# Kernel tuning notes

Hardware: AMD Instinct MI355X
Metric: run time of the kernel (lower is better)

## Reference

```python
import jax, jax.numpy as jnp
import numpy as np
from math import sqrt

N = 50000
E = 800000
D_EMB = 512
DK = 64
DV = 64
HEADS = 8


def setup_inputs() -> dict:
    key = jax.random.key(0)
    k1, k2, k3, k4 = jax.random.split(key, 4)
    x = jax.random.normal(k1, (N, D_EMB), dtype=jnp.float32)
    edge_index = jax.random.randint(k2, (2, E), 0, N, dtype=jnp.int64)
    out_qkv = (2 * DK + DV) * HEADS  # 1536
    W_qkv = jax.random.normal(k3, (out_qkv, D_EMB), dtype=jnp.float32) / sqrt(D_EMB)
    b_qkv = jnp.zeros((out_qkv,), dtype=jnp.float32)
    W_ff = jax.random.normal(k4, (D_EMB, DV * HEADS), dtype=jnp.float32) / sqrt(DV * HEADS)
    b_ff = jnp.zeros((D_EMB,), dtype=jnp.float32)
    return {"x": x, "edge_index": edge_index, "W_qkv": W_qkv, "b_qkv": b_qkv,
            "W_ff": W_ff, "b_ff": b_ff}


def _attention_message(Q, K, V, senders, receivers, n_nodes):
    # Q,K: [N, H, dK], V: [N, H, dV]; edge lists: [E]
    scale = 1.0 / sqrt(Q.shape[-1])
    # per-edge scores: [E, H]
    scores = jnp.einsum('ehd,ehd->eh', Q[receivers], K[senders]) * scale
    # segment softmax over incoming edges of each receiver
    smax = jax.ops.segment_max(scores, receivers, num_segments=n_nodes)  # [N, H]
    ex = jnp.exp(scores - smax[receivers])                               # [E, H]
    denom = jax.ops.segment_sum(ex, receivers, num_segments=n_nodes)    # [N, H]
    att = ex / denom[receivers]                                         # [E, H]
    # weighted scatter of V from senders to receivers: [N, H, dV]
    out = jax.ops.segment_sum(att[:, :, None] * V[senders], receivers,
                              num_segments=n_nodes)
    return out, att


def reference(x, edge_index, W_qkv, b_qkv, W_ff, b_ff):
    n_nodes = x.shape[0]
    qkv = x @ W_qkv.T + b_qkv  # [N, (2*dK+dV)*H]
    Q, K, V = jnp.split(qkv, [DK * HEADS, 2 * DK * HEADS], axis=-1)
    Q = Q.reshape(n_nodes, HEADS, DK)
    K = K.reshape(n_nodes, HEADS, DK)
    V = V.reshape(n_nodes, HEADS, DV)
    senders, receivers = edge_index[0], edge_index[1]
    msg, _ = _attention_message(Q, K, V, senders, receivers, n_nodes)
    # aggregate_heads: flatten heads and project to d_Embedding
    out = msg.reshape(n_nodes, HEADS * DV) @ W_ff.T + b_ff
    return out
```

## Files before the change

kernel.cpp:

```cpp
#include <hip/hip_runtime.h>

static constexpr int NN = 50000;
static constexpr int NE = 800000;
static constexpr int DEMB = 512;
static constexpr int QKV_OUT = 1536;

typedef _Float16 half8 __attribute__((ext_vector_type(8)));
typedef float floatx4 __attribute__((ext_vector_type(4)));

#define KQ_SCALE (127.0f / 5.5f)
#define KQ_DEQ   (5.5f / 127.0f)

static constexpr size_t OFF_QH   = 0;
static constexpr size_t OFF_VH   = 51200000;
static constexpr size_t OFF_K8   = 102400000;
static constexpr size_t OFF_MSG  = 153600000;
static constexpr size_t OFF_SRT  = 204800000;
static constexpr size_t OFF_DEG  = 208000000;
static constexpr size_t OFF_OFFA = 208200000;
static constexpr size_t OFF_CUR  = 208400064;
static constexpr size_t OFF_FLAG = 208600064;
static constexpr size_t OFF_WQH  = 208600128;
static constexpr size_t OFF_WFH  = 210172992;

typedef __attribute__((address_space(1))) const void* gas_ptr;
typedef __attribute__((address_space(3))) void* lds_ptr_t;

__device__ __forceinline__ void load_lds16(const void* g, void* l) {
  __builtin_amdgcn_global_load_lds((gas_ptr)g, (lds_ptr_t)l, 16, 0, 0);
}

__global__ __launch_bounds__(256)
void k_cvt(const float* __restrict__ in, _Float16* __restrict__ out, int n8) {
  int i = blockIdx.x * 256 + threadIdx.x;
  if (i < n8) {
    floatx4 a = *(const floatx4*)(in + (size_t)i * 8);
    floatx4 b = *(const floatx4*)(in + (size_t)i * 8 + 4);
    half8 h;
    #pragma unroll
    for (int q = 0; q < 4; ++q) { h[q] = (_Float16)a[q]; h[q + 4] = (_Float16)b[q]; }
    *(half8*)(out + (size_t)i * 8) = h;
  }
}

__global__ __launch_bounds__(64)
void k_detect64(const void* __restrict__ edge, int* __restrict__ flag) {
  if (threadIdx.x == 0) {
    const int* p = (const int*)edge;
    int is64 = 1;
    for (int i = 0; i < 16; ++i) if (p[2 * i + 1] != 0) is64 = 0;
    *flag = is64;
  }
}

__device__ __forceinline__ int edge_at(const void* edge, int row, int e, int is64) {
  if (is64) return (int)((const long long*)edge)[(size_t)row * NE + e];
  return ((const int*)edge)[(size_t)row * NE + e];
}

__global__ __launch_bounds__(256)
void k_histo(const void* __restrict__ edge, const int* __restrict__ flag,
             int* __restrict__ deg) {
  int e = blockIdx.x * 256 + threadIdx.x;
  if (e < NE) {
    int r = edge_at(edge, 1, e, *flag);
    atomicAdd(&deg[r], 1);
  }
}

__global__ __launch_bounds__(1024)
void k_scan(const int* __restrict__ deg, int* __restrict__ off,
            int* __restrict__ cur, int n) {
  __shared__ int sums[1024];
  int tid = threadIdx.x;
  int per = (n + 1023) >> 10;
  int start = tid * per;
  int end = start + per; if (end > n) end = n;
  int s = 0;
  for (int i = start; i < end; ++i) s += deg[i];
  sums[tid] = s;
  __syncthreads();
  for (int d = 1; d < 1024; d <<= 1) {
    int v = (tid >= d) ? sums[tid - d] : 0;
    __syncthreads();
    sums[tid] += v;
    __syncthreads();
  }
  int run = (tid == 0) ? 0 : sums[tid - 1];
  for (int i = start; i < end; ++i) {
    off[i] = run; cur[i] = run; run += deg[i];
  }
  if (tid == 0) off[n] = sums[1023];
}

__global__ __launch_bounds__(256)
void k_scatter(const void* __restrict__ edge, const int* __restrict__ flag,
               int* __restrict__ cur, int* __restrict__ srt) {
  int e = blockIdx.x * 256 + threadIdx.x;
  if (e < NE) {
    int is64 = *flag;
    int r = edge_at(edge, 1, e, is64);
    int s = edge_at(edge, 0, e, is64);
    int pos = atomicAdd(&cur[r], 1);
    srt[pos] = s;
  }
}

template<int MODE>
__global__ __launch_bounds__(256)
void k_gemm_nt(const _Float16* __restrict__ Ah, const _Float16* __restrict__ Bh,
               const float* __restrict__ bias,
               void* __restrict__ out0, void* __restrict__ out1, void* __restrict__ out2,
               int M, int N, int K) {
  __shared__ _Float16 As[128 * 32];
  __shared__ _Float16 Bs[128 * 32];
  const int tid = threadIdx.x;
  const int m0 = blockIdx.x * 128;
  const int n0 = blockIdx.y * 128;
  const int wid = tid >> 6, lane = tid & 63;
  const int wr = wid >> 1, wc = wid & 1;

  floatx4 acc[4][4];
  #pragma unroll
  for (int i = 0; i < 4; ++i)
    #pragma unroll
    for (int j = 0; j < 4; ++j)
      #pragma unroll
      for (int q = 0; q < 4; ++q) acc[i][j][q] = 0.f;

  const int srow = tid >> 2;
  const int sslot = tid & 3;
  const int fr = lane & 15;
  const int fslot = lane >> 4;

  int garow0 = m0 + srow;       if (garow0 >= M) garow0 = M - 1;
  int garow1 = m0 + srow + 64;  if (garow1 >= M) garow1 = M - 1;
  const int aslot0 = sslot ^ (srow & 3);
  const int gbrow0 = n0 + srow, gbrow1 = n0 + srow + 64;

  for (int k0 = 0; k0 < K; k0 += 32) {
    load_lds16(Ah + (size_t)garow0 * K + k0 + aslot0 * 8, (char*)As + wid * 1024);
    load_lds16(Ah + (size_t)garow1 * K + k0 + aslot0 * 8, (char*)As + 4096 + wid * 1024);
    load_lds16(Bh + (size_t)gbrow0 * K + k0 + aslot0 * 8, (char*)Bs + wid * 1024);
    load_lds16(Bh + (size_t)gbrow1 * K + k0 + aslot0 * 8, (char*)Bs + 4096 + wid * 1024);
    __syncthreads();

    half8 a[4], b[4];
    #pragma unroll
    for (int m = 0; m < 4; ++m) {
      int R = wr * 64 + m * 16 + fr;
      a[m] = *(const half8*)(As + R * 32 + ((fslot ^ (R & 3)) << 3));
    }
    #pragma unroll
    for (int n = 0; n < 4; ++n) {
      int R = wc * 64 + n * 16 + fr;
      b[n] = *(const half8*)(Bs + R * 32 + ((fslot ^ (R & 3)) << 3));
    }
    #pragma unroll
    for (int m = 0; m < 4; ++m)
      #pragma unroll
      for (int n = 0; n < 4; ++n)
        acc[m][n] = __builtin_amdgcn_mfma_f32_16x16x32_f16(a[m], b[n], acc[m][n], 0, 0, 0);
    __syncthreads();
  }

  const int fq = (lane >> 4) << 2;
  #pragma unroll
  for (int m = 0; m < 4; ++m) {
    #pragma unroll
    for (int n = 0; n < 4; ++n) {
      int gn = n0 + wc * 64 + n * 16 + fr;
      float bv = bias[gn];
      #pragma unroll
      for (int q = 0; q < 4; ++q) {
        int gm = m0 + wr * 64 + m * 16 + fq + q;
        if (gm < M) {
          float val = acc[m][n][q] + bv;
          if (MODE == 0) {
            int region = gn >> 9;
            int col = gn & 511;
            size_t idx = (size_t)gm * 512 + col;
            if (region == 0)      ((_Float16*)out0)[idx] = (_Float16)val;
            else if (region == 1) {
              float s = fminf(fmaxf(val * KQ_SCALE, -127.f), 127.f);
              ((signed char*)out1)[idx] = (signed char)__float2int_rn(s);
            }
            else                  ((_Float16*)out2)[idx] = (_Float16)val;
          } else {
            ((float*)out0)[(size_t)gm * N + gn] = val;
          }
        }
      }
    }
  }
}

__global__ __launch_bounds__(256)
void k_attn(const _Float16* __restrict__ Qh, const signed char* __restrict__ K8,
            const _Float16* __restrict__ Vh, const int* __restrict__ off,
            const int* __restrict__ srt, _Float16* __restrict__ msg) {
  int r = blockIdx.x * 4 + (threadIdx.x >> 6);
  if (r >= NN) return;
  int lane = threadIdx.x & 63;
  int h = lane >> 3, j = lane & 7;
  int qoff = h * 64 + j * 8;

  half8 qh = *(const half8*)(Qh + (size_t)r * 512 + qoff);
  float q[8];
  #pragma unroll
  for (int i = 0; i < 8; ++i) q[i] = (float)qh[i] * 0.125f * KQ_DEQ;

  float denom = 0.f;
  float acc[8];
  #pragma unroll
  for (int i = 0; i < 8; ++i) acc[i] = 0.f;

  int e0 = off[r], e1 = off[r + 1];
  if (e1 <= e0) {
    half8 z = {};
    *(half8*)(msg + (size_t)r * 512 + qoff) = z;
    return;
  }

  auto gload = [&](uint2& k8, half8& vh, int s) {
    k8 = *(const uint2*)(K8 + (size_t)s * 512 + qoff);
    vh = *(const half8*)(Vh + (size_t)s * 512 + qoff);
  };
  auto consume = [&](uint2 k8, half8 vh) {
    int xw = (int)k8.x, yw = (int)k8.y;
    float p = 0.f;
    p += q[0] * (float)((xw << 24) >> 24);
    p += q[1] * (float)((xw << 16) >> 24);
    p += q[2] * (float)((xw << 8) >> 24);
    p += q[3] * (float)(xw >> 24);
    p += q[4] * (float)((yw << 24) >> 24);
    p += q[5] * (float)((yw << 16) >> 24);
    p += q[6] * (float)((yw << 8) >> 24);
    p += q[7] * (float)(yw >> 24);
    p += __shfl_xor(p, 1);
    p += __shfl_xor(p, 2);
    p += __shfl_xor(p, 4);
    float w = __expf(p);
    denom += w;
    #pragma unroll
    for (int i = 0; i < 8; ++i) acc[i] += w * (float)vh[i];
  };
  auto sidx = [&](int e) { return srt[e < e1 ? e : e1 - 1]; };

  uint2 kb0, kb1, kb2, kb3;
  half8 vb0, vb1, vb2, vb3;
  gload(kb0, vb0, sidx(e0));
  gload(kb1, vb1, sidx(e0 + 1));
  gload(kb2, vb2, sidx(e0 + 2));
  gload(kb3, vb3, sidx(e0 + 3));
  int sn0 = sidx(e0 + 4), sn1 = sidx(e0 + 5), sn2 = sidx(e0 + 6), sn3 = sidx(e0 + 7);

  int e = e0;
  for (; e + 4 <= e1; e += 4) {
    consume(kb0, vb0); gload(kb0, vb0, sn0);
    consume(kb1, vb1); gload(kb1, vb1, sn1);
    consume(kb2, vb2); gload(kb2, vb2, sn2);
    consume(kb3, vb3); gload(kb3, vb3, sn3);
    sn0 = sidx(e + 8); sn1 = sidx(e + 9); sn2 = sidx(e + 10); sn3 = sidx(e + 11);
  }
  int rem = e1 - e;
  if (rem > 0) consume(kb0, vb0);
  if (rem > 1) consume(kb1, vb1);
  if (rem > 2) consume(kb2, vb2);

  float inv = 1.f / denom;
  half8 oh;
  #pragma unroll
  for (int i = 0; i < 8; ++i) oh[i] = (_Float16)(acc[i] * inv);
  *(half8*)(msg + (size_t)r * 512 + qoff) = oh;
}

extern "C" void kernel_launch(void* const* d_in, const int* in_sizes, int n_in,
                              void* d_out, int out_size, void* d_ws, size_t ws_size,
                              hipStream_t stream) {
  const float* x     = (const float*)d_in[0];
  const void*  edge  = d_in[1];
  const float* W_qkv = (const float*)d_in[2];
  const float* b_qkv = (const float*)d_in[3];
  const float* W_ff  = (const float*)d_in[4];
  const float* b_ff  = (const float*)d_in[5];
  float* out = (float*)d_out;

  char* ws = (char*)d_ws;
  _Float16* Qh = (_Float16*)(ws + OFF_QH);
  _Float16* Vh = (_Float16*)(ws + OFF_VH);
  signed char* K8 = (signed char*)(ws + OFF_K8);
  _Float16* msgb = (_Float16*)(ws + OFF_MSG);
  _Float16* xh   = (_Float16*)(ws + OFF_MSG);
  int* srt  = (int*)(ws + OFF_SRT);
  int* deg  = (int*)(ws + OFF_DEG);
  int* offa = (int*)(ws + OFF_OFFA);
  int* cur  = (int*)(ws + OFF_CUR);
  int* flag = (int*)(ws + OFF_FLAG);
  _Float16* wqh = (_Float16*)(ws + OFF_WQH);
  _Float16* wfh = (_Float16*)(ws + OFF_WFH);

  hipMemsetAsync(deg, 0, NN * sizeof(int), stream);
  k_detect64<<<1, 64, 0, stream>>>(edge, flag);

  k_cvt<<<(NN * DEMB / 8 + 255) / 256, 256, 0, stream>>>(x, xh, NN * DEMB / 8);
  k_cvt<<<(QKV_OUT * DEMB / 8 + 255) / 256, 256, 0, stream>>>(W_qkv, wqh, QKV_OUT * DEMB / 8);
  k_cvt<<<(DEMB * DEMB / 8 + 255) / 256, 256, 0, stream>>>(W_ff, wfh, DEMB * DEMB / 8);

  k_gemm_nt<0><<<dim3(391, 12), 256, 0, stream>>>(
      xh, wqh, b_qkv, Qh, K8, Vh, NN, QKV_OUT, DEMB);

  k_histo<<<(NE + 255) / 256, 256, 0, stream>>>(edge, flag, deg);
  k_scan<<<1, 1024, 0, stream>>>(deg, offa, cur, NN);
  k_scatter<<<(NE + 255) / 256, 256, 0, stream>>>(edge, flag, cur, srt);

  k_attn<<<(NN + 3) / 4, 256, 0, stream>>>(Qh, K8, Vh, offa, srt, msgb);

  k_gemm_nt<1><<<dim3(391, 4), 256, 0, stream>>>(
      msgb, wfh, b_ff, out, nullptr, nullptr, NN, DEMB, DEMB);
}
```

Measured before the change: 651.3 us.

## Quantize V to int8, swap GEMM grid axes, and change LDS swizzle

Stores V as int8 with the same fixed scale as K, which halves the gathered V bytes per edge in the attention kernel. The dequant factor is folded into the final normalization. The GEMM grid is transposed so blocks sharing an A row tile run next to each other, which should improve L2 reuse of the activations. The LDS XOR swizzle now uses (row>>1)&3 to cut bank conflicts. The int8 V with a fixed clamp range adds quantization error and relies on V values staying inside that range.

```diff
diff --git a/kernel.cpp b/kernel.cpp
--- a/kernel.cpp
+++ b/kernel.cpp
@@ -12,16 +12,16 @@
 #define KQ_DEQ   (5.5f / 127.0f)
 
 static constexpr size_t OFF_QH   = 0;
-static constexpr size_t OFF_VH   = 51200000;
-static constexpr size_t OFF_K8   = 102400000;
-static constexpr size_t OFF_MSG  = 153600000;
-static constexpr size_t OFF_SRT  = 204800000;
-static constexpr size_t OFF_DEG  = 208000000;
-static constexpr size_t OFF_OFFA = 208200000;
-static constexpr size_t OFF_CUR  = 208400064;
-static constexpr size_t OFF_FLAG = 208600064;
-static constexpr size_t OFF_WQH  = 208600128;
-static constexpr size_t OFF_WFH  = 210172992;
+static constexpr size_t OFF_K8   = 51200000;
+static constexpr size_t OFF_V8   = 76800000;
+static constexpr size_t OFF_MSG  = 102400000;
+static constexpr size_t OFF_SRT  = 153600000;
+static constexpr size_t OFF_DEG  = 156800000;
+static constexpr size_t OFF_OFFA = 157000000;
+static constexpr size_t OFF_CUR  = 157200064;
+static constexpr size_t OFF_FLAG = 157400064;
+static constexpr size_t OFF_WQH  = 157400128;
+static constexpr size_t OFF_WFH  = 158972992;
 
 typedef __attribute__((address_space(1))) const void* gas_ptr;
 typedef __attribute__((address_space(3))) void* lds_ptr_t;
@@ -115,8 +115,8 @@
   __shared__ _Float16 As[128 * 32];
   __shared__ _Float16 Bs[128 * 32];
   const int tid = threadIdx.x;
-  const int m0 = blockIdx.x * 128;
-  const int n0 = blockIdx.y * 128;
+  const int m0 = blockIdx.y * 128;
+  const int n0 = blockIdx.x * 128;
   const int wid = tid >> 6, lane = tid & 63;
   const int wr = wid >> 1, wc = wid & 1;
 
@@ -135,26 +135,27 @@
 
   int garow0 = m0 + srow;       if (garow0 >= M) garow0 = M - 1;
   int garow1 = m0 + srow + 64;  if (garow1 >= M) garow1 = M - 1;
-  const int aslot0 = sslot ^ (srow & 3);
+  const int asl0 = sslot ^ ((srow >> 1) & 3);
+  const int asl1 = sslot ^ (((srow + 64) >> 1) & 3);
   const int gbrow0 = n0 + srow, gbrow1 = n0 + srow + 64;
 
   for (int k0 = 0; k0 < K; k0 += 32) {
-    load_lds16(Ah + (size_t)garow0 * K + k0 + aslot0 * 8, (char*)As + wid * 1024);
-    load_lds16(Ah + (size_t)garow1 * K + k0 + aslot0 * 8, (char*)As + 4096 + wid * 1024);
-    load_lds16(Bh + (size_t)gbrow0 * K + k0 + aslot0 * 8, (char*)Bs + wid * 1024);
-    load_lds16(Bh + (size_t)gbrow1 * K + k0 + aslot0 * 8, (char*)Bs + 4096 + wid * 1024);
+    load_lds16(Ah + (size_t)garow0 * K + k0 + asl0 * 8, (char*)As + wid * 1024);
+    load_lds16(Ah + (size_t)garow1 * K + k0 + asl1 * 8, (char*)As + 4096 + wid * 1024);
+    load_lds16(Bh + (size_t)gbrow0 * K + k0 + asl0 * 8, (char*)Bs + wid * 1024);
+    load_lds16(Bh + (size_t)gbrow1 * K + k0 + asl1 * 8, (char*)Bs + 4096 + wid * 1024);
     __syncthreads();
 
     half8 a[4], b[4];
     #pragma unroll
     for (int m = 0; m < 4; ++m) {
       int R = wr * 64 + m * 16 + fr;
-      a[m] = *(const half8*)(As + R * 32 + ((fslot ^ (R & 3)) << 3));
+      a[m] = *(const half8*)(As + R * 32 + ((fslot ^ ((R >> 1) & 3)) << 3));
     }
     #pragma unroll
     for (int n = 0; n < 4; ++n) {
       int R = wc * 64 + n * 16 + fr;
-      b[n] = *(const half8*)(Bs + R * 32 + ((fslot ^ (R & 3)) << 3));
+      b[n] = *(const half8*)(Bs + R * 32 + ((fslot ^ ((R >> 1) & 3)) << 3));
     }
     #pragma unroll
     for (int m = 0; m < 4; ++m)
@@ -180,12 +181,13 @@
             int region = gn >> 9;
             int col = gn & 511;
             size_t idx = (size_t)gm * 512 + col;
-            if (region == 0)      ((_Float16*)out0)[idx] = (_Float16)val;
-            else if (region == 1) {
+            if (region == 0) ((_Float16*)out0)[idx] = (_Float16)val;
+            else {
               float s = fminf(fmaxf(val * KQ_SCALE, -127.f), 127.f);
-              ((signed char*)out1)[idx] = (signed char)__float2int_rn(s);
+              signed char c = (signed char)__float2int_rn(s);
+              if (region == 1) ((signed char*)out1)[idx] = c;
+              else             ((signed char*)out2)[idx] = c;
             }
-            else                  ((_Float16*)out2)[idx] = (_Float16)val;
           } else {
             ((float*)out0)[(size_t)gm * N + gn] = val;
           }
@@ -197,7 +199,7 @@
 
 __global__ __launch_bounds__(256)
 void k_attn(const _Float16* __restrict__ Qh, const signed char* __restrict__ K8,
-            const _Float16* __restrict__ Vh, const int* __restrict__ off,
+            const signed char* __restrict__ V8, const int* __restrict__ off,
             const int* __restrict__ srt, _Float16* __restrict__ msg) {
   int r = blockIdx.x * 4 + (threadIdx.x >> 6);
   if (r >= NN) return;
@@ -222,11 +224,11 @@
     return;
   }
 
-  auto gload = [&](uint2& k8, half8& vh, int s) {
+  auto gload = [&](uint2& k8, uint2& v8, int s) {
     k8 = *(const uint2*)(K8 + (size_t)s * 512 + qoff);
-    vh = *(const half8*)(Vh + (size_t)s * 512 + qoff);
+    v8 = *(const uint2*)(V8 + (size_t)s * 512 + qoff);
   };
-  auto consume = [&](uint2 k8, half8 vh) {
+  auto consume = [&](uint2 k8, uint2 v8) {
     int xw = (int)k8.x, yw = (int)k8.y;
     float p = 0.f;
     p += q[0] * (float)((xw << 24) >> 24);
@@ -242,13 +244,19 @@
     p += __shfl_xor(p, 4);
     float w = __expf(p);
     denom += w;
-    #pragma unroll
-    for (int i = 0; i < 8; ++i) acc[i] += w * (float)vh[i];
+    int vx = (int)v8.x, vy = (int)v8.y;
+    acc[0] += w * (float)((vx << 24) >> 24);
+    acc[1] += w * (float)((vx << 16) >> 24);
+    acc[2] += w * (float)((vx << 8) >> 24);
+    acc[3] += w * (float)(vx >> 24);
+    acc[4] += w * (float)((vy << 24) >> 24);
+    acc[5] += w * (float)((vy << 16) >> 24);
+    acc[6] += w * (float)((vy << 8) >> 24);
+    acc[7] += w * (float)(vy >> 24);
   };
   auto sidx = [&](int e) { return srt[e < e1 ? e : e1 - 1]; };
 
-  uint2 kb0, kb1, kb2, kb3;
-  half8 vb0, vb1, vb2, vb3;
+  uint2 kb0, kb1, kb2, kb3, vb0, vb1, vb2, vb3;
   gload(kb0, vb0, sidx(e0));
   gload(kb1, vb1, sidx(e0 + 1));
   gload(kb2, vb2, sidx(e0 + 2));
@@ -268,7 +276,7 @@
   if (rem > 1) consume(kb1, vb1);
   if (rem > 2) consume(kb2, vb2);
 
-  float inv = 1.f / denom;
+  float inv = KQ_DEQ / denom;
   half8 oh;
   #pragma unroll
   for (int i = 0; i < 8; ++i) oh[i] = (_Float16)(acc[i] * inv);
@@ -288,8 +296,8 @@
 
   char* ws = (char*)d_ws;
   _Float16* Qh = (_Float16*)(ws + OFF_QH);
-  _Float16* Vh = (_Float16*)(ws + OFF_VH);
   signed char* K8 = (signed char*)(ws + OFF_K8);
+  signed char* V8 = (signed char*)(ws + OFF_V8);
   _Float16* msgb = (_Float16*)(ws + OFF_MSG);
   _Float16* xh   = (_Float16*)(ws + OFF_MSG);
   int* srt  = (int*)(ws + OFF_SRT);
@@ -307,15 +315,15 @@
   k_cvt<<<(QKV_OUT * DEMB / 8 + 255) / 256, 256, 0, stream>>>(W_qkv, wqh, QKV_OUT * DEMB / 8);
   k_cvt<<<(DEMB * DEMB / 8 + 255) / 256, 256, 0, stream>>>(W_ff, wfh, DEMB * DEMB / 8);
 
-  k_gemm_nt<0><<<dim3(391, 12), 256, 0, stream>>>(
-      xh, wqh, b_qkv, Qh, K8, Vh, NN, QKV_OUT, DEMB);
+  k_gemm_nt<0><<<dim3(12, 391), 256, 0, stream>>>(
+      xh, wqh, b_qkv, Qh, K8, V8, NN, QKV_OUT, DEMB);
 
   k_histo<<<(NE + 255) / 256, 256, 0, stream>>>(edge, flag, deg);
   k_scan<<<1, 1024, 0, stream>>>(deg, offa, cur, NN);
   k_scatter<<<(NE + 255) / 256, 256, 0, stream>>>(edge, flag, cur, srt);
 
-  k_attn<<<(NN + 3) / 4, 256, 0, stream>>>(Qh, K8, Vh, offa, srt, msgb);
-
-  k_gemm_nt<1><<<dim3(391, 4), 256, 0, stream>>>(
+  k_attn<<<(NN + 3) / 4, 256, 0, stream>>>(Qh, K8, V8, offa, srt, msgb);
+
+  k_gemm_nt<1><<<dim3(4, 391), 256, 0, stream>>>(
       msgb, wfh, b_ff, out, nullptr, nullptr, NN, DEMB, DEMB);
 }
```

Result: faster. 598.0 us (-8.2%).
